# Optimization experiments

Hardware: AMD Instinct MI355X
Metric: run time of the kernel (lower is better)

The kernel has to match this reference:

```python
import jax, jax.numpy as jnp
import numpy as np

N_NODES = 50000


def gcn_layer(x, src, dst, ew, W, b, n_nodes):
    # PyG GCNConv: add self-loops (weight 1), symmetric deg^-1/2 normalization,
    # linear transform, scatter-add aggregation at destination, then bias.
    loop = jnp.arange(n_nodes, dtype=src.dtype)
    s = jnp.concatenate([src, loop])
    d = jnp.concatenate([dst, loop])
    w = jnp.concatenate([ew, jnp.ones((n_nodes,), dtype=ew.dtype)])
    deg = jax.ops.segment_sum(w, d, num_segments=n_nodes)  # [N]
    dinv = jnp.where(deg > 0, jax.lax.rsqrt(jnp.where(deg > 0, deg, 1.0)), 0.0)
    norm = dinv[s] * w * dinv[d]  # [E+N]
    h = x @ W  # [N, out]
    msg = h[s] * norm[:, None]  # gather + scale, [E+N, out]
    out = jax.ops.segment_sum(msg, d, num_segments=n_nodes)  # scatter-add
    return out + b


def setup_inputs() -> dict:
    key = jax.random.key(0)
    k1, k2, k3, k4, k5, k6, k7 = jax.random.split(key, 7)
    N, E, C_IN, C_OUT = N_NODES, 600000, 128, 128
    x = jax.random.normal(k1, (N, C_IN), dtype=jnp.float32)
    edge_index = jax.random.randint(k2, (2, E), 0, N, dtype=jnp.int64)
    edge_weight = jax.random.uniform(k3, (E,), dtype=jnp.float32)
    # Glorot-style init like PyG's Linear default
    s1 = 1.0 / np.sqrt(C_IN)
    s2 = 1.0 / np.sqrt(C_OUT)
    W1 = jax.random.uniform(k4, (C_IN, C_OUT), jnp.float32, -s1, s1)
    b1 = jnp.zeros((C_OUT,), dtype=jnp.float32)
    W2 = jax.random.uniform(k5, (C_OUT, C_OUT), jnp.float32, -s2, s2)
    b2 = jnp.zeros((C_OUT,), dtype=jnp.float32)
    return {"x": x, "edge_index": edge_index, "edge_weight": edge_weight,
            "W1": W1, "b1": b1, "W2": W2, "b2": b2}


def reference(x, edge_index, edge_weight, W1, b1, W2, b2):
    src, dst = edge_index[0], edge_index[1]
    h = jax.nn.relu(gcn_layer(x, src, dst, edge_weight, W1, b1, N_NODES))
    return jax.nn.relu(gcn_layer(h, src, dst, edge_weight, W2, b2, N_NODES))
```

## Files before the change

kernel.cpp:

```cpp
#include <hip/hip_runtime.h>
#include <math.h>

#define CH   128
#define CH4  32
#define TPB  256
#define SCANB 1024
#define WIMG 16384
#define NREP 8
#define FIXS 1048576.0f

typedef __attribute__((ext_vector_type(8))) short short8;
typedef __attribute__((ext_vector_type(4))) float floatx4;
typedef __attribute__((ext_vector_type(8))) float float8;
typedef unsigned long long u64;

static __device__ __forceinline__ unsigned short f2bf(float f) {
    unsigned u = __float_as_uint(f);
    return (unsigned short)((u + 0x7fffu + ((u >> 16) & 1u)) >> 16);
}
static __device__ __forceinline__ float bf2f(unsigned short s) {
    return __uint_as_float(((unsigned)s) << 16);
}
static __device__ __forceinline__ float8 bf8_to_f8(short8 u) {
    float8 f;
    #pragma unroll
    for (int i = 0; i < 8; ++i) f[i] = bf2f((unsigned short)u[i]);
    return f;
}

__global__ void k_prep(const float* __restrict__ W1, const float* __restrict__ W2,
                       short* __restrict__ Wsplit, float4* __restrict__ zbase,
                       int nzero4, int nbPrep) {
    int bx = blockIdx.x;
    if (bx >= nbPrep) {
        int i = (bx - nbPrep) * TPB + threadIdx.x;
        if (i < nzero4) zbase[i] = make_float4(0.f, 0.f, 0.f, 0.f);
        return;
    }
    int i = bx * TPB + threadIdx.x;
    if (i >= 2 * CH * CH) return;
    int layer = i >> 14;
    int idx   = i & 16383;
    int k = idx >> 7, c = idx & 127;
    float w = (layer ? W2 : W1)[k * CH + c];
    unsigned short hi = f2bf(w);
    unsigned short lo = f2bf(w - bf2f(hi));
    int colh = c >> 6, nn = c & 63;
    int kt = k >> 5, q = (k & 31) >> 3, j = k & 7;
    int ns = nn >> 4, ln = q * 16 + (nn & 15);
    size_t base = (size_t)(layer * 2 + colh) * WIMG;
    size_t off  = ((size_t)(kt * 4 + ns) * 64 + ln) * 8 + j;
    Wsplit[base + off]        = (short)hi;
    Wsplit[base + 8192 + off] = (short)lo;
}

static __device__ __forceinline__ void gemm_body_f32(
        const float* __restrict__ X, const short* __restrict__ Wfrag,
        unsigned short* __restrict__ H, int n, int tile, int colh, int tid) {
    __shared__ __align__(16) short sW[2][4][4][64][8];
    {
        const float4* gsrc = (const float4*)Wfrag;
        float4* ldst = (float4*)sW;
        #pragma unroll
        for (int i = 0; i < 8; ++i)
            ldst[i * TPB + tid] = gsrc[i * TPB + tid];
    }
    __syncthreads();

    const int lane = tid & 63;
    const int wv   = tid >> 6;
    const int q    = lane >> 4;
    const int m    = lane & 15;
    const int row0 = tile * 64 + wv * 16;
    if (row0 >= n) return;

    int rrow = row0 + m;
    if (rrow > n - 1) rrow = n - 1;

    const float4* xr = (const float4*)(X + (size_t)rrow * CH);
    float4 xa[4][2];
    #pragma unroll
    for (int kt = 0; kt < 4; ++kt) {
        xa[kt][0] = xr[kt * 8 + q * 2 + 0];
        xa[kt][1] = xr[kt * 8 + q * 2 + 1];
    }

    floatx4 acc[4];
    #pragma unroll
    for (int ns = 0; ns < 4; ++ns) acc[ns] = (floatx4){0.f, 0.f, 0.f, 0.f};

    #pragma unroll
    for (int kt = 0; kt < 4; ++kt) {
        float xf[8] = { xa[kt][0].x, xa[kt][0].y, xa[kt][0].z, xa[kt][0].w,
                        xa[kt][1].x, xa[kt][1].y, xa[kt][1].z, xa[kt][1].w };
        short8 ah, al;
        #pragma unroll
        for (int j = 0; j < 8; ++j) {
            float v = xf[j];
            unsigned short h = f2bf(v);
            ah[j] = (short)h;
            al[j] = (short)f2bf(v - bf2f(h));
        }
        #pragma unroll
        for (int ns = 0; ns < 4; ++ns) {
            short8 bh = *(const short8*)&sW[0][kt][ns][lane][0];
            short8 bl = *(const short8*)&sW[1][kt][ns][lane][0];
            acc[ns] = __builtin_amdgcn_mfma_f32_16x16x32_bf16(ah, bh, acc[ns], 0, 0, 0);
            acc[ns] = __builtin_amdgcn_mfma_f32_16x16x32_bf16(al, bh, acc[ns], 0, 0, 0);
            acc[ns] = __builtin_amdgcn_mfma_f32_16x16x32_bf16(ah, bl, acc[ns], 0, 0, 0);
        }
    }

    #pragma unroll
    for (int ns = 0; ns < 4; ++ns) {
        #pragma unroll
        for (int reg = 0; reg < 4; ++reg) {
            int r = row0 + q * 4 + reg;
            if (r < n)
                H[(size_t)r * CH + colh * 64 + ns * 16 + m] = f2bf(acc[ns][reg]);
        }
    }
}

__global__ __launch_bounds__(TPB, 4)
void k_gemm_rank(const float* __restrict__ X, const short* __restrict__ Wsplit,
                 unsigned short* __restrict__ H, int n,
                 const int* __restrict__ dst, const float* __restrict__ ew,
                 u64* __restrict__ counts_rep, int* __restrict__ rank,
                 int E, int nbE4, int Np) {
    int bx = blockIdx.x;
    if (bx < nbE4) {
        int stride = nbE4 * TPB;
        int e = bx * TPB + threadIdx.x;
        #pragma unroll
        for (int it = 0; it < 4; ++it, e += stride) {
            if (e < E) {
                int d = dst[e];
                if ((unsigned)d < (unsigned)n) {
                    int rep = e & (NREP - 1);
                    u64 pk = (1ull << 40) |
                             (u64)(unsigned)__float2uint_rn(ew[e] * FIXS);
                    u64 old = atomicAdd(&counts_rep[(size_t)rep * Np + d], pk);
                    rank[e] = (int)(old >> 40);
                }
            }
        }
    } else {
        bx -= nbE4;
        int colh = bx & 1;
        gemm_body_f32(X, Wsplit + (size_t)colh * WIMG, H, n, bx >> 1, colh,
                      threadIdx.x);
    }
}

__global__ __launch_bounds__(TPB, 4)
void k_gemm_bf(const unsigned short* __restrict__ X, const short* __restrict__ Wsplit,
               unsigned short* __restrict__ H, int n) {
    __shared__ __align__(16) short sW[4][4][64][8];
    const int tid  = threadIdx.x;
    const int colh = (int)blockIdx.x & 1;
    const int tile = (int)blockIdx.x >> 1;
    {
        const float4* gsrc = (const float4*)(Wsplit + (size_t)colh * WIMG);
        float4* ldst = (float4*)sW;
        #pragma unroll
        for (int i = 0; i < 4; ++i)
            ldst[i * TPB + tid] = gsrc[i * TPB + tid];
    }
    __syncthreads();

    const int lane = tid & 63;
    const int wv   = tid >> 6;
    const int q    = lane >> 4;
    const int m    = lane & 15;
    const int row0 = tile * 64 + wv * 16;
    if (row0 >= n) return;

    int rrow = row0 + m;
    if (rrow > n - 1) rrow = n - 1;

    const short8* xr8 = (const short8*)(X + (size_t)rrow * CH);
    short8 a[4];
    #pragma unroll
    for (int kt = 0; kt < 4; ++kt) a[kt] = xr8[kt * 4 + q];

    floatx4 acc[4];
    #pragma unroll
    for (int ns = 0; ns < 4; ++ns) acc[ns] = (floatx4){0.f, 0.f, 0.f, 0.f};

    #pragma unroll
    for (int kt = 0; kt < 4; ++kt) {
        #pragma unroll
        for (int ns = 0; ns < 4; ++ns) {
            short8 bh = *(const short8*)&sW[kt][ns][lane][0];
            acc[ns] = __builtin_amdgcn_mfma_f32_16x16x32_bf16(a[kt], bh, acc[ns], 0, 0, 0);
        }
    }

    #pragma unroll
    for (int ns = 0; ns < 4; ++ns) {
        #pragma unroll
        for (int reg = 0; reg < 4; ++reg) {
            int r = row0 + q * 4 + reg;
            if (r < n)
                H[(size_t)r * CH + colh * 64 + ns * 16 + m] = f2bf(acc[ns][reg]);
        }
    }
}

__global__ __launch_bounds__(SCANB)
void k_scan1(const u64* __restrict__ counts_rep, int Np,
             int* __restrict__ counts_tot, int* __restrict__ repoff8,
             int* __restrict__ row_start, float* __restrict__ dinv,
             int* __restrict__ partials, int* __restrict__ pp_s,
             int* __restrict__ done, int nb, int n) {
    __shared__ int s[SCANB];
    __shared__ int slast;
    int gid = blockIdx.x * SCANB + threadIdx.x;
    int c[NREP];
    int v = 0;
    u64 wsum = 0;
    #pragma unroll
    for (int r = 0; r < NREP; ++r) {
        u64 pk = (gid < n) ? counts_rep[(size_t)r * Np + gid] : 0ull;
        c[r] = (int)(pk >> 40);
        wsum += pk & ((1ull << 40) - 1);
        v += c[r];
    }
    s[threadIdx.x] = v;
    __syncthreads();
    for (int off = 1; off < SCANB; off <<= 1) {
        int t = (threadIdx.x >= off) ? s[threadIdx.x - off] : 0;
        __syncthreads();
        s[threadIdx.x] += t;
        __syncthreads();
    }
    if (gid < n) {
        row_start[gid]  = s[threadIdx.x] - v;
        counts_tot[gid] = v;
        dinv[gid] = rsqrtf(1.0f + (float)wsum * (1.0f / FIXS));
        int pre = 0;
        int ro[NREP];
        #pragma unroll
        for (int r = 0; r < NREP; ++r) { ro[r] = pre; pre += c[r]; }
        ((int4*)repoff8)[gid * 2 + 0] = make_int4(ro[0], ro[1], ro[2], ro[3]);
        ((int4*)repoff8)[gid * 2 + 1] = make_int4(ro[4], ro[5], ro[6], ro[7]);
    }
    if (threadIdx.x == SCANB - 1) {
        partials[blockIdx.x] = s[SCANB - 1];
        __threadfence();
        int old = atomicAdd(done, 1);
        slast = (old == nb - 1);
    }
    __syncthreads();
    if (slast && threadIdx.x < 64) {
        int pv = (threadIdx.x < nb) ? atomicAdd(&partials[threadIdx.x], 0) : 0;
        int inc = pv;
        #pragma unroll
        for (int off = 1; off < 64; off <<= 1) {
            int t = __shfl_up(inc, off, 64);
            if ((threadIdx.x & 63) >= off) inc += t;
        }
        if (threadIdx.x < nb) pp_s[threadIdx.x] = inc - pv;
    }
}

__global__ void k_fill(const int* __restrict__ src, const int* __restrict__ dst,
                       const float* __restrict__ ew, const int* __restrict__ row_start,
                       const int* __restrict__ pp_s, const int* __restrict__ repoff8,
                       const int* __restrict__ rank, const float* __restrict__ dinv,
                       int2* __restrict__ edges, int E, int n) {
    int e = blockIdx.x * blockDim.x + threadIdx.x;
    if (e >= E) return;
    int s = src[e], d = dst[e];
    if ((unsigned)s >= (unsigned)n || (unsigned)d >= (unsigned)n) return;
    int rep = e & (NREP - 1);
    int base = row_start[d] + pp_s[d >> 10] + repoff8[d * NREP + rep];
    edges[base + rank[e]] = make_int2(s, __float_as_int(ew[e] * dinv[s]));
}

static __device__ __forceinline__ float8 agg_node8(
        const short8* __restrict__ h8, const int2* __restrict__ edges,
        float di, const float8 b, int node, int tx,
        const int* __restrict__ row_start, const int* __restrict__ pp_s,
        const int* __restrict__ counts) {
    float8 hv = bf8_to_f8(h8[(size_t)node * 16 + tx]);
    float8 acc;
    #pragma unroll
    for (int i = 0; i < 8; ++i) acc[i] = 0.f;

    int j   = row_start[node] + pp_s[node >> 10];
    int end = j + counts[node];

    for (; j + 8 <= end; j += 8) {
        int2 e[8];
        #pragma unroll
        for (int i = 0; i < 8; ++i) e[i] = edges[j + i];
        short8 g[8];
        #pragma unroll
        for (int i = 0; i < 8; ++i) g[i] = h8[(size_t)e[i].x * 16 + tx];
        #pragma unroll
        for (int i = 0; i < 8; ++i) {
            float w = __int_as_float(e[i].y);
            float8 gf = bf8_to_f8(g[i]);
            #pragma unroll
            for (int c = 0; c < 8; ++c) acc[c] += gf[c] * w;
        }
    }
    if (j + 4 <= end) {
        int2 e[4];
        #pragma unroll
        for (int i = 0; i < 4; ++i) e[i] = edges[j + i];
        short8 g[4];
        #pragma unroll
        for (int i = 0; i < 4; ++i) g[i] = h8[(size_t)e[i].x * 16 + tx];
        #pragma unroll
        for (int i = 0; i < 4; ++i) {
            float w = __int_as_float(e[i].y);
            float8 gf = bf8_to_f8(g[i]);
            #pragma unroll
            for (int c = 0; c < 8; ++c) acc[c] += gf[c] * w;
        }
        j += 4;
    }
    for (; j < end; ++j) {
        int2 e0 = edges[j];
        float w0 = __int_as_float(e0.y);
        float8 gf = bf8_to_f8(h8[(size_t)e0.x * 16 + tx]);
        #pragma unroll
        for (int c = 0; c < 8; ++c) acc[c] += gf[c] * w0;
    }

    float di2 = di * di;
    float8 o;
    #pragma unroll
    for (int c = 0; c < 8; ++c) o[c] = di2 * hv[c] + di * acc[c] + b[c];
    return o;
}

__global__ __launch_bounds__(TPB)
void k_aggregate1(const unsigned short* __restrict__ h,
                  const int* __restrict__ row_start, const int* __restrict__ pp_s,
                  const int* __restrict__ counts, const int2* __restrict__ edges,
                  const float* __restrict__ dinv, const float* __restrict__ bias,
                  unsigned short* __restrict__ out, int n) {
    int t = blockIdx.x * blockDim.x + threadIdx.x;
    int node = t >> 4;
    if (node >= n) return;
    int tx = t & 15;
    float8 b;
    #pragma unroll
    for (int c = 0; c < 8; ++c) b[c] = bias[tx * 8 + c];
    float8 o = agg_node8((const short8*)h, edges, dinv[node], b, node, tx,
                         row_start, pp_s, counts);
    short8 u;
    #pragma unroll
    for (int c = 0; c < 8; ++c) u[c] = (short)f2bf(fmaxf(o[c], 0.f));
    ((short8*)out)[(size_t)node * 16 + tx] = u;
}

__global__ __launch_bounds__(TPB)
void k_aggregate2(const unsigned short* __restrict__ h,
                  const int* __restrict__ row_start, const int* __restrict__ pp_s,
                  const int* __restrict__ counts, const int2* __restrict__ edges,
                  const float* __restrict__ dinv, const float* __restrict__ bias,
                  float* __restrict__ out, int n) {
    int t = blockIdx.x * blockDim.x + threadIdx.x;
    int node = t >> 4;
    if (node >= n) return;
    int tx = t & 15;
    float8 b;
    #pragma unroll
    for (int c = 0; c < 8; ++c) b[c] = bias[tx * 8 + c];
    float8 o = agg_node8((const short8*)h, edges, dinv[node], b, node, tx,
                         row_start, pp_s, counts);
    float4 lo = make_float4(fmaxf(o[0], 0.f), fmaxf(o[1], 0.f),
                            fmaxf(o[2], 0.f), fmaxf(o[3], 0.f));
    float4 hi = make_float4(fmaxf(o[4], 0.f), fmaxf(o[5], 0.f),
                            fmaxf(o[6], 0.f), fmaxf(o[7], 0.f));
    ((float4*)out)[(size_t)node * CH4 + tx * 2 + 0] = lo;
    ((float4*)out)[(size_t)node * CH4 + tx * 2 + 1] = hi;
}

extern "C" void kernel_launch(void* const* d_in, const int* in_sizes, int n_in,
                              void* d_out, int out_size, void* d_ws, size_t ws_size,
                              hipStream_t stream) {
    const float* x  = (const float*)d_in[0];
    const int*   ei = (const int*)d_in[1];
    const float* ew = (const float*)d_in[2];
    const float* W1 = (const float*)d_in[3];
    const float* b1 = (const float*)d_in[4];
    const float* W2 = (const float*)d_in[5];
    const float* b2 = (const float*)d_in[6];
    float* out = (float*)d_out;

    const int N = in_sizes[0] / CH;
    const int E = in_sizes[2];
    const int* src = ei;
    const int* dst = ei + E;

    size_t Np = ((size_t)N + 255) & ~(size_t)255;
    size_t Ep = ((size_t)E + 63) & ~(size_t)63;
    float* ws          = (float*)d_ws;
    float* dinv        = ws;
    unsigned short* h  = (unsigned short*)(dinv + Np);
    unsigned short* o1 = h + (size_t)N * CH;
    unsigned short* h2 = o1 + (size_t)N * CH;
    u64*   counts_rep  = (u64*)(h2 + (size_t)N * CH);
    int*   done        = (int*)(counts_rep + NREP * Np);
    int    nzero4      = (int)((2 * NREP * Np + 64) / 4);
    int*  counts_tot   = done + 64;
    int*  row_start    = counts_tot + Np;
    int*  repoff8      = row_start + Np;
    int*  rank         = repoff8 + NREP * Np;
    int*  partials     = rank + Ep;
    int*  pp_s         = partials + 64;
    int2* edges        = (int2*)(pp_s + 64);
    short* Wsplit      = (short*)(edges + E);

    const int nbE    = (E + TPB - 1) / TPB;
    const int nbE4   = (E + TPB * 4 - 1) / (TPB * 4);
    const int nbAgg  = (int)(((size_t)N * 16 + TPB - 1) / TPB);
    const int nbScan = (N + SCANB - 1) / SCANB;
    const int nbGemm2 = 2 * ((N + 63) / 64);
    const int nbPrep  = (2 * CH * CH + TPB - 1) / TPB;
    const int nbZero  = (nzero4 + TPB - 1) / TPB;

    k_prep     <<<nbPrep + nbZero, TPB, 0, stream>>>(W1, W2, Wsplit,
                                                     (float4*)counts_rep,
                                                     nzero4, nbPrep);

    k_gemm_rank<<<nbE4 + nbGemm2, TPB, 0, stream>>>(x, Wsplit, h, N, dst, ew,
                                                    counts_rep, rank, E, nbE4,
                                                    (int)Np);
    k_scan1    <<<nbScan, SCANB, 0, stream>>>(counts_rep, (int)Np, counts_tot,
                                              repoff8, row_start, dinv,
                                              partials, pp_s, done, nbScan, N);
    k_fill     <<<nbE, TPB, 0, stream>>>(src, dst, ew, row_start, pp_s, repoff8,
                                         rank, dinv, edges, E, N);

    k_aggregate1<<<nbAgg, TPB, 0, stream>>>(h, row_start, pp_s, counts_tot,
                                            edges, dinv, b1, o1, N);
    k_gemm_bf   <<<nbGemm2, TPB, 0, stream>>>(o1, Wsplit + 2 * (size_t)WIMG,
                                              h2, N);
    k_aggregate2<<<nbAgg, TPB, 0, stream>>>(h2, row_start, pp_s, counts_tot,
                                            edges, dinv, b2, out, N);
}
```

Baseline: 210.3 us.

## Fuse layer-1 aggregation with layer-2 GEMM through an LDS tile

Merges the first aggregation kernel and the second bf16 MFMA GEMM into one kernel. Each block aggregates 64 nodes into a padded shared-memory tile, then multiplies it by the full W2 held in LDS. This removes one launch and the write and re-read of the intermediate activation buffer. In exchange each block carries 32 KB of W2 plus the tile in LDS, which limits occupancy, and only a quarter as many threads run the latency-bound gather (each handles four nodes in sequence).

```diff
diff --git a/kernel.cpp b/kernel.cpp
--- a/kernel.cpp
+++ b/kernel.cpp
@@ -153,61 +153,6 @@
     }
 }
 
-__global__ __launch_bounds__(TPB, 4)
-void k_gemm_bf(const unsigned short* __restrict__ X, const short* __restrict__ Wsplit,
-               unsigned short* __restrict__ H, int n) {
-    __shared__ __align__(16) short sW[4][4][64][8];
-    const int tid  = threadIdx.x;
-    const int colh = (int)blockIdx.x & 1;
-    const int tile = (int)blockIdx.x >> 1;
-    {
-        const float4* gsrc = (const float4*)(Wsplit + (size_t)colh * WIMG);
-        float4* ldst = (float4*)sW;
-        #pragma unroll
-        for (int i = 0; i < 4; ++i)
-            ldst[i * TPB + tid] = gsrc[i * TPB + tid];
-    }
-    __syncthreads();
-
-    const int lane = tid & 63;
-    const int wv   = tid >> 6;
-    const int q    = lane >> 4;
-    const int m    = lane & 15;
-    const int row0 = tile * 64 + wv * 16;
-    if (row0 >= n) return;
-
-    int rrow = row0 + m;
-    if (rrow > n - 1) rrow = n - 1;
-
-    const short8* xr8 = (const short8*)(X + (size_t)rrow * CH);
-    short8 a[4];
-    #pragma unroll
-    for (int kt = 0; kt < 4; ++kt) a[kt] = xr8[kt * 4 + q];
-
-    floatx4 acc[4];
-    #pragma unroll
-    for (int ns = 0; ns < 4; ++ns) acc[ns] = (floatx4){0.f, 0.f, 0.f, 0.f};
-
-    #pragma unroll
-    for (int kt = 0; kt < 4; ++kt) {
-        #pragma unroll
-        for (int ns = 0; ns < 4; ++ns) {
-            short8 bh = *(const short8*)&sW[kt][ns][lane][0];
-            acc[ns] = __builtin_amdgcn_mfma_f32_16x16x32_bf16(a[kt], bh, acc[ns], 0, 0, 0);
-        }
-    }
-
-    #pragma unroll
-    for (int ns = 0; ns < 4; ++ns) {
-        #pragma unroll
-        for (int reg = 0; reg < 4; ++reg) {
-            int r = row0 + q * 4 + reg;
-            if (r < n)
-                H[(size_t)r * CH + colh * 64 + ns * 16 + m] = f2bf(acc[ns][reg]);
-        }
-    }
-}
-
 __global__ __launch_bounds__(SCANB)
 void k_scan1(const u64* __restrict__ counts_rep, int Np,
              int* __restrict__ counts_tot, int* __restrict__ repoff8,
@@ -339,24 +284,89 @@
 }
 
 __global__ __launch_bounds__(TPB)
-void k_aggregate1(const unsigned short* __restrict__ h,
-                  const int* __restrict__ row_start, const int* __restrict__ pp_s,
-                  const int* __restrict__ counts, const int2* __restrict__ edges,
-                  const float* __restrict__ dinv, const float* __restrict__ bias,
-                  unsigned short* __restrict__ out, int n) {
-    int t = blockIdx.x * blockDim.x + threadIdx.x;
-    int node = t >> 4;
-    if (node >= n) return;
-    int tx = t & 15;
+void k_agg_gemm(const unsigned short* __restrict__ h,
+                const int* __restrict__ row_start, const int* __restrict__ pp_s,
+                const int* __restrict__ counts, const int2* __restrict__ edges,
+                const float* __restrict__ dinv, const float* __restrict__ bias,
+                const short* __restrict__ W2img,
+                unsigned short* __restrict__ h2, int n) {
+    __shared__ __align__(16) short sW[2][4][4][64][8];
+    __shared__ __align__(16) short8 tile[64 * 17];
+    const int tid = threadIdx.x;
+    {
+        float4* ldst = (float4*)sW;
+        #pragma unroll
+        for (int i = 0; i < 8; ++i) {
+            int idx = i * TPB + tid;
+            int colh = idx >> 10;
+            int within = idx & 1023;
+            ldst[idx] = ((const float4*)(W2img + (size_t)colh * WIMG))[within];
+        }
+    }
+
+    const int bnode0 = (int)blockIdx.x * 64;
+    const int tx = tid & 15;
+    const int tg = tid >> 4;
     float8 b;
     #pragma unroll
     for (int c = 0; c < 8; ++c) b[c] = bias[tx * 8 + c];
-    float8 o = agg_node8((const short8*)h, edges, dinv[node], b, node, tx,
-                         row_start, pp_s, counts);
-    short8 u;
-    #pragma unroll
-    for (int c = 0; c < 8; ++c) u[c] = (short)f2bf(fmaxf(o[c], 0.f));
-    ((short8*)out)[(size_t)node * 16 + tx] = u;
+    #pragma unroll
+    for (int rr = 0; rr < 4; ++rr) {
+        int nl = rr * 16 + tg;
+        int node = bnode0 + nl;
+        short8 u;
+        if (node < n) {
+            float8 o = agg_node8((const short8*)h, edges, dinv[node], b, node,
+                                 tx, row_start, pp_s, counts);
+            #pragma unroll
+            for (int c = 0; c < 8; ++c) u[c] = (short)f2bf(fmaxf(o[c], 0.f));
+        } else {
+            #pragma unroll
+            for (int c = 0; c < 8; ++c) u[c] = 0;
+        }
+        tile[nl * 17 + tx] = u;
+    }
+    __syncthreads();
+
+    const int lane = tid & 63;
+    const int wv   = tid >> 6;
+    const int q    = lane >> 4;
+    const int m    = lane & 15;
+    short8 a[4];
+    #pragma unroll
+    for (int kt = 0; kt < 4; ++kt)
+        a[kt] = tile[(wv * 16 + m) * 17 + kt * 4 + q];
+
+    floatx4 acc[2][4];
+    #pragma unroll
+    for (int ch = 0; ch < 2; ++ch)
+        #pragma unroll
+        for (int ns = 0; ns < 4; ++ns) acc[ch][ns] = (floatx4){0.f, 0.f, 0.f, 0.f};
+
+    #pragma unroll
+    for (int kt = 0; kt < 4; ++kt) {
+        #pragma unroll
+        for (int ch = 0; ch < 2; ++ch) {
+            #pragma unroll
+            for (int ns = 0; ns < 4; ++ns) {
+                short8 bh = *(const short8*)&sW[ch][kt][ns][lane][0];
+                acc[ch][ns] = __builtin_amdgcn_mfma_f32_16x16x32_bf16(
+                                  a[kt], bh, acc[ch][ns], 0, 0, 0);
+            }
+        }
+    }
+
+    #pragma unroll
+    for (int ch = 0; ch < 2; ++ch)
+        #pragma unroll
+        for (int ns = 0; ns < 4; ++ns)
+            #pragma unroll
+            for (int reg = 0; reg < 4; ++reg) {
+                int r = bnode0 + wv * 16 + q * 4 + reg;
+                if (r < n)
+                    h2[(size_t)r * CH + ch * 64 + ns * 16 + m] =
+                        f2bf(acc[ch][ns][reg]);
+            }
 }
 
 __global__ __launch_bounds__(TPB)
@@ -404,8 +414,7 @@
     float* ws          = (float*)d_ws;
     float* dinv        = ws;
     unsigned short* h  = (unsigned short*)(dinv + Np);
-    unsigned short* o1 = h + (size_t)N * CH;
-    unsigned short* h2 = o1 + (size_t)N * CH;
+    unsigned short* h2 = h + (size_t)N * CH;
     u64*   counts_rep  = (u64*)(h2 + (size_t)N * CH);
     int*   done        = (int*)(counts_rep + NREP * Np);
     int    nzero4      = (int)((2 * NREP * Np + 64) / 4);
@@ -422,27 +431,27 @@
     const int nbE4   = (E + TPB * 4 - 1) / (TPB * 4);
     const int nbAgg  = (int)(((size_t)N * 16 + TPB - 1) / TPB);
     const int nbScan = (N + SCANB - 1) / SCANB;
-    const int nbGemm2 = 2 * ((N + 63) / 64);
-    const int nbPrep  = (2 * CH * CH + TPB - 1) / TPB;
-    const int nbZero  = (nzero4 + TPB - 1) / TPB;
+    const int nbGemm = 2 * ((N + 63) / 64);
+    const int nbAG   = (N + 63) / 64;
+    const int nbPrep = (2 * CH * CH + TPB - 1) / TPB;
+    const int nbZero = (nzero4 + TPB - 1) / TPB;
 
     k_prep     <<<nbPrep + nbZero, TPB, 0, stream>>>(W1, W2, Wsplit,
                                                      (float4*)counts_rep,
                                                      nzero4, nbPrep);
 
-    k_gemm_rank<<<nbE4 + nbGemm2, TPB, 0, stream>>>(x, Wsplit, h, N, dst, ew,
-                                                    counts_rep, rank, E, nbE4,
-                                                    (int)Np);
+    k_gemm_rank<<<nbE4 + nbGemm, TPB, 0, stream>>>(x, Wsplit, h, N, dst, ew,
+                                                   counts_rep, rank, E, nbE4,
+                                                   (int)Np);
     k_scan1    <<<nbScan, SCANB, 0, stream>>>(counts_rep, (int)Np, counts_tot,
                                               repoff8, row_start, dinv,
                                               partials, pp_s, done, nbScan, N);
     k_fill     <<<nbE, TPB, 0, stream>>>(src, dst, ew, row_start, pp_s, repoff8,
                                          rank, dinv, edges, E, N);
 
-    k_aggregate1<<<nbAgg, TPB, 0, stream>>>(h, row_start, pp_s, counts_tot,
-                                            edges, dinv, b1, o1, N);
-    k_gemm_bf   <<<nbGemm2, TPB, 0, stream>>>(o1, Wsplit + 2 * (size_t)WIMG,
-                                              h2, N);
+    k_agg_gemm <<<nbAG, TPB, 0, stream>>>(h, row_start, pp_s, counts_tot,
+                                          edges, dinv, b1,
+                                          Wsplit + 2 * (size_t)WIMG, h2, N);
     k_aggregate2<<<nbAgg, TPB, 0, stream>>>(h2, row_start, pp_s, counts_tot,
                                             edges, dinv, b2, out, N);
 }
```

After: 217.7 us. 3.5% more time.
